# Optimization experiments

Measured on AMD Instinct MI355X. Metric: run time of the kernel, lower is better.

## Reference

```python
import jax, jax.numpy as jnp
import numpy as np

DIM = 2048
K_DIM = 2048
Q_HEADS = 16
KV_HEADS = 4
HEAD_DIM = DIM // Q_HEADS  # 128
KV_DIM = HEAD_DIM * KV_HEADS  # 512
MAX_LEN = 2048
ROPE_THETA = 10000.0
ROPE_FACTOR = 8.0


def _rope_cos_sin(seq_len):
    # Faithful to generate_sin_cos_pos_emb with is_causal=True
    d = HEAD_DIM
    seq_eff = max(seq_len, MAX_LEN)
    base_adj = (ROPE_FACTOR * seq_eff / MAX_LEN - (ROPE_FACTOR - 1.0)) ** (d / (d - 2))
    adjusted_base = ROPE_THETA * base_adj
    inv_freq = 1.0 / adjusted_base ** (np.arange(0, d, 2, dtype=np.float32) / d)
    pos = np.arange(seq_len, dtype=np.float32)  # causal: no centering
    freqs = pos[:, None] * inv_freq[None, :]            # [S, d/2]
    emb = np.concatenate([freqs, freqs], axis=-1)        # [S, d]
    return jnp.asarray(np.cos(emb), jnp.float32), jnp.asarray(np.sin(emb), jnp.float32)


def _rotate_half(x):
    x1, x2 = jnp.split(x, 2, axis=-1)
    return jnp.concatenate([-x2, x1], axis=-1)


def setup_inputs() -> dict:
    key = jax.random.key(0)
    ks = jax.random.split(key, 12)
    B, S = 1, 2048
    s_in = 1.0 / np.sqrt(DIM)
    s_k = 1.0 / np.sqrt(K_DIM)
    return {
        "query": jax.random.normal(ks[0], (B, S, DIM), jnp.float32),
        "key": jax.random.normal(ks[1], (B, S, K_DIM), jnp.float32),
        "value": jax.random.normal(ks[2], (B, S, K_DIM), jnp.float32),
        "Wq": jax.random.uniform(ks[3], (DIM, DIM), jnp.float32, -s_in, s_in),
        "bq": jax.random.uniform(ks[4], (DIM,), jnp.float32, -s_in, s_in),
        "Wk": jax.random.uniform(ks[5], (KV_DIM, K_DIM), jnp.float32, -s_k, s_k),
        "bk": jax.random.uniform(ks[6], (KV_DIM,), jnp.float32, -s_k, s_k),
        "Wv": jax.random.uniform(ks[7], (KV_DIM, K_DIM), jnp.float32, -s_k, s_k),
        "bv": jax.random.uniform(ks[8], (KV_DIM,), jnp.float32, -s_k, s_k),
        "Wo": jax.random.uniform(ks[9], (DIM, DIM), jnp.float32, -s_in, s_in),
        "bo": jax.random.uniform(ks[10], (DIM,), jnp.float32, -s_in, s_in),
    }


def reference(query, key, value, Wq, bq, Wk, bk, Wv, bv, Wo, bo):
    B, S, _ = query.shape
    scale = HEAD_DIM ** -0.5

    q = query @ Wq.T + bq                                   # [B,S,DIM]
    k = key @ Wk.T + bk                                     # [B,S,KV_DIM]
    v = value @ Wv.T + bv                                   # [B,S,KV_DIM]

    q = q.reshape(B, S, Q_HEADS, HEAD_DIM)
    k = k.reshape(B, S, KV_HEADS, HEAD_DIM)
    v = v.reshape(B, S, KV_HEADS, HEAD_DIM)

    cos, sin = _rope_cos_sin(S)                              # [S,D]
    cos = cos[None, :, None, :]
    sin = sin[None, :, None, :]
    q = q * cos + _rotate_half(q) * sin
    k = k * cos + _rotate_half(k) * sin

    # [B,H,S,D]
    q = q.transpose(0, 2, 1, 3)
    k = k.transpose(0, 2, 1, 3)
    v = v.transpose(0, 2, 1, 3)

    rep = Q_HEADS // KV_HEADS
    k = jnp.repeat(k, rep, axis=1)
    v = jnp.repeat(v, rep, axis=1)

    scores = jnp.einsum('bhqd,bhkd->bhqk', q, k) * scale
    causal = jnp.tril(jnp.ones((S, S), bool))
    scores = jnp.where(causal[None, None], scores, jnp.finfo(scores.dtype).min)
    attn = jax.nn.softmax(scores, axis=-1)
    out = jnp.einsum('bhqk,bhkd->bhqd', attn, v)             # [B,H,S,D]

    out = out.transpose(0, 2, 1, 3).reshape(B, S, DIM)
    return out @ Wo.T + bo
```

## Files before the change

kernel.cpp:

```cpp
#include <hip/hip_runtime.h>
#include <stdint.h>

typedef __attribute__((ext_vector_type(8))) short short8;
typedef __attribute__((ext_vector_type(4))) float f32x4;
typedef __attribute__((ext_vector_type(4))) unsigned short u16x4;
typedef unsigned short bf16_t;

__device__ __forceinline__ bf16_t f2bf(float f) {
  union { float f; uint32_t u; } x; x.f = f;
  uint32_t r = x.u + 0x7fffu + ((x.u >> 16) & 1u);
  return (bf16_t)(r >> 16);
}

__device__ __forceinline__ void ld_g2l_16(const bf16_t* g, bf16_t* l) {
  __builtin_amdgcn_global_load_lds(
      (const __attribute__((address_space(1))) void*)g,
      (__attribute__((address_space(3))) void*)l, 16, 0, 0);
}

__global__ void rope_tab(float* __restrict__ CS, float* __restrict__ SN) {
  int idx = blockIdx.x * 256 + threadIdx.x;
  int i = idx & 63, pos = idx >> 6;
  float ang = (float)pos * exp2f((float)i * -0.2076205059f);
  CS[idx] = cosf(ang);
  SN[idx] = sinf(ang);
}

__global__ void convert_all(const float* __restrict__ s0, const float* __restrict__ s1,
                            const float* __restrict__ s2, const float* __restrict__ s3,
                            const float* __restrict__ s4, const float* __restrict__ s5,
                            const float* __restrict__ s6,
                            bf16_t* __restrict__ d0, bf16_t* __restrict__ d1,
                            bf16_t* __restrict__ d2, bf16_t* __restrict__ d3,
                            bf16_t* __restrict__ d4, bf16_t* __restrict__ d5,
                            bf16_t* __restrict__ d6) {
  int i = blockIdx.x * 256 + threadIdx.x;
  const float* src; bf16_t* dst; int off;
  if (i < 5 * 1048576) {
    int t = i >> 20; off = i & 1048575;
    if (t == 0)      { src = s0; dst = d0; }
    else if (t == 1) { src = s1; dst = d1; }
    else if (t == 2) { src = s2; dst = d2; }
    else if (t == 3) { src = s3; dst = d3; }
    else             { src = s4; dst = d4; }
  } else {
    int j = i - 5 * 1048576;
    if (j < 262144) { src = s5; dst = d5; off = j; }
    else            { src = s6; dst = d6; off = j - 262144; }
  }
  f32x4 v = *(const f32x4*)(src + (size_t)off * 4);
  u16x4 o;
  o[0] = f2bf(v[0]); o[1] = f2bf(v[1]); o[2] = f2bf(v[2]); o[3] = f2bf(v[3]);
  *(u16x4*)(dst + (size_t)off * 4) = o;
}

template <int MODE>
__device__ __forceinline__ void gemm_core(
    bf16_t* __restrict__ As, bf16_t* __restrict__ Bs,
    const bf16_t* __restrict__ A, const bf16_t* __restrict__ Bm,
    const float* __restrict__ bias, void* __restrict__ Cout,
    int N, int K, int m0, int n0,
    const float* __restrict__ CS, const float* __restrict__ SN) {
  const int tid = threadIdx.x;
  const int lane = tid & 63, quad = lane >> 4, l16 = lane & 15;
  const int wv = tid >> 6;
  const int m_off = wv * 32;
  const int c0 = tid, c1 = tid + 256;
  const int r0 = c0 >> 2, col0 = (c0 & 3) * 8;
  const int r1 = c1 >> 2, col1 = (c1 & 3) * 8;

  f32x4 acc[2][8];
  const f32x4 zf = {0.f, 0.f, 0.f, 0.f};
#pragma unroll
  for (int mi = 0; mi < 2; ++mi)
#pragma unroll
    for (int ni = 0; ni < 8; ++ni) acc[mi][ni] = zf;

  const bf16_t* Ap0 = A + (size_t)(m0 + r0) * K + col0;
  const bf16_t* Ap1 = A + (size_t)(m0 + r1) * K + col1;
  const bf16_t* Bp0 = Bm + (size_t)(n0 + r0) * K + col0;
  const bf16_t* Bp1 = Bm + (size_t)(n0 + r1) * K + col1;
  bf16_t* lA0 = As + c0 * 8;  bf16_t* lA1 = As + c1 * 8;
  bf16_t* lB0 = Bs + c0 * 8;  bf16_t* lB1 = Bs + c1 * 8;

  for (int k0 = 0; k0 < K; k0 += 32) {
    ld_g2l_16(Ap0 + k0, lA0);
    ld_g2l_16(Ap1 + k0, lA1);
    ld_g2l_16(Bp0 + k0, lB0);
    ld_g2l_16(Bp1 + k0, lB1);
    __syncthreads();
    short8 af[2], bf[8];
#pragma unroll
    for (int mi = 0; mi < 2; ++mi)
      af[mi] = *(const short8*)(&As[(m_off + mi * 16 + l16) * 32 + quad * 8]);
#pragma unroll
    for (int ni = 0; ni < 8; ++ni)
      bf[ni] = *(const short8*)(&Bs[(ni * 16 + l16) * 32 + quad * 8]);
#pragma unroll
    for (int mi = 0; mi < 2; ++mi)
#pragma unroll
      for (int ni = 0; ni < 8; ++ni)
        acc[mi][ni] = __builtin_amdgcn_mfma_f32_16x16x32_bf16(
            af[mi], bf[ni], acc[mi][ni], 0, 0, 0);
    __syncthreads();
  }

  if (MODE == 0 || MODE == 2) {
#pragma unroll
    for (int mi = 0; mi < 2; ++mi)
#pragma unroll
      for (int ni = 0; ni < 8; ++ni) {
        int n = n0 + ni * 16 + l16;
        int mbase = m0 + m_off + mi * 16 + quad * 4;
        float bv = bias[n];
#pragma unroll
        for (int r = 0; r < 4; ++r) {
          float v = acc[mi][ni][r] + bv;
          int m = mbase + r;
          if (MODE == 0) ((float*)Cout)[(size_t)m * N + n] = v;
          else           ((bf16_t*)Cout)[(size_t)n * 2048 + m] = f2bf(v);
        }
      }
  } else {
    const float scale = (MODE == 3) ? 0.08838834764831845f : 1.0f;
    bf16_t* dst = (bf16_t*)Cout;
#pragma unroll
    for (int mi = 0; mi < 2; ++mi)
#pragma unroll
      for (int r = 0; r < 4; ++r) {
        int m = m0 + m_off + mi * 16 + quad * 4 + r;
#pragma unroll
        for (int ni = 0; ni < 4; ++ni) {
          int i = ni * 16 + l16;
          int n_lo = n0 + i;
          float v1 = acc[mi][ni][r] + bias[n_lo];
          float v2 = acc[mi][ni + 4][r] + bias[n_lo + 64];
          float c = CS[m * 64 + i];
          float s = SN[m * 64 + i];
          float o1 = (v1 * c - v2 * s) * scale;
          float o2 = (v2 * c + v1 * s) * scale;
          dst[(size_t)m * N + n_lo] = f2bf(o1);
          dst[(size_t)m * N + n_lo + 64] = f2bf(o2);
        }
      }
  }
}

__global__ __launch_bounds__(256) void gemm_qkv(
    const bf16_t* __restrict__ qb, const bf16_t* __restrict__ kb,
    const bf16_t* __restrict__ vb, const bf16_t* __restrict__ wqb,
    const bf16_t* __restrict__ wkb, const bf16_t* __restrict__ wvb,
    const float* __restrict__ bq, const float* __restrict__ bk,
    const float* __restrict__ bv, bf16_t* __restrict__ Qr,
    bf16_t* __restrict__ Kr, bf16_t* __restrict__ Vt,
    const float* __restrict__ CS, const float* __restrict__ SN) {
  __shared__ __align__(16) bf16_t As[128 * 32];
  __shared__ __align__(16) bf16_t Bs[128 * 32];
  int bx = blockIdx.x, m0 = blockIdx.y * 128;
  if (bx < 16)
    gemm_core<3>(As, Bs, qb, wqb, bq, Qr, 2048, 2048, m0, bx * 128, CS, SN);
  else if (bx < 20)
    gemm_core<4>(As, Bs, kb, wkb, bk, Kr, 512, 2048, m0, (bx - 16) * 128, CS, SN);
  else
    gemm_core<2>(As, Bs, vb, wvb, bv, Vt, 512, 2048, m0, (bx - 20) * 128, CS, SN);
}

__global__ __launch_bounds__(256) void gemm_o(
    const bf16_t* __restrict__ Ob, const bf16_t* __restrict__ wob,
    const float* __restrict__ bo, float* __restrict__ out) {
  __shared__ __align__(16) bf16_t As[128 * 32];
  __shared__ __align__(16) bf16_t Bs[128 * 32];
  gemm_core<0>(As, Bs, Ob, wob, bo, out, 2048, 2048,
               blockIdx.y * 128, blockIdx.x * 128, nullptr, nullptr);
}

__global__ __launch_bounds__(256, 2) void attn_fwd(
    const bf16_t* __restrict__ Qr, const bf16_t* __restrict__ Kr,
    const bf16_t* __restrict__ Vt, bf16_t* __restrict__ Oo) {
  const int h = blockIdx.y;
  const int qt = 31 - blockIdx.x;
  const int tid = threadIdx.x;
  const int wv = tid >> 6, lane = tid & 63, quad = lane >> 4, l16 = lane & 15;
  const int q_base = qt * 64 + wv * 16;
  const int hkv = h >> 2;
  const int qg = q_base + l16;

  __shared__ __align__(16) bf16_t Ks[64 * 136];
  __shared__ __align__(16) bf16_t Vs[128 * 72];
  __shared__ __align__(16) float Sb[4][16 * 66];
  float* mys = Sb[wv];

  short8 qf[4];
  {
    const bf16_t* qp = Qr + (size_t)(q_base + l16) * 2048 + h * 128 + quad * 8;
#pragma unroll
    for (int kc = 0; kc < 4; ++kc) qf[kc] = *(const short8*)(qp + kc * 32);
  }

  const f32x4 zf = {0.f, 0.f, 0.f, 0.f};
  f32x4 o[8];
#pragma unroll
  for (int di = 0; di < 8; ++di) o[di] = zf;
  float l_acc = 0.f;

  const int ntiles = qt + 1;
  for (int t = 0; t < ntiles; ++t) {
    const int k0 = t * 64;
#pragma unroll
    for (int j = 0; j < 4; ++j) {
      int cid = tid + j * 256;
      int row = cid >> 4, c = cid & 15;
      f32x4 tmp = *(const f32x4*)(&Kr[(size_t)(k0 + row) * 512 + hkv * 128 + c * 8]);
      *(f32x4*)(&Ks[row * 136 + c * 8]) = tmp;
    }
#pragma unroll
    for (int j = 0; j < 4; ++j) {
      int cid = tid + j * 256;
      int row = cid >> 3, c = cid & 7;
      f32x4 tmp = *(const f32x4*)(&Vt[(size_t)(hkv * 128 + row) * 2048 + k0 + c * 8]);
      *(f32x4*)(&Vs[row * 72 + c * 8]) = tmp;
    }
    __syncthreads();

    f32x4 sacc[4];
#pragma unroll
    for (int sub = 0; sub < 4; ++sub) sacc[sub] = zf;
#pragma unroll
    for (int sub = 0; sub < 4; ++sub)
#pragma unroll
      for (int kc = 0; kc < 4; ++kc) {
        short8 kf = *(const short8*)(&Ks[(sub * 16 + l16) * 136 + kc * 32 + quad * 8]);
        sacc[sub] = __builtin_amdgcn_mfma_f32_16x16x32_bf16(qf[kc], kf, sacc[sub], 0, 0, 0);
      }
#pragma unroll
    for (int sub = 0; sub < 4; ++sub)
#pragma unroll
      for (int r = 0; r < 4; ++r)
        mys[(quad * 4 + r) * 66 + sub * 16 + l16] = sacc[sub][r];
    __asm__ volatile("s_waitcnt lgkmcnt(0)" ::: "memory");
    const float* rp = mys + l16 * 66 + quad * 8;
    float p0[8], p1[8];
    if (k0 + 63 > q_base) {
#pragma unroll
      for (int j = 0; j < 8; ++j) {
        int kg = k0 + quad * 8 + j;
        p0[j] = (kg <= qg) ? __expf(rp[j]) : 0.f;
        p1[j] = (kg + 32 <= qg) ? __expf(rp[32 + j]) : 0.f;
      }
    } else {
#pragma unroll
      for (int j = 0; j < 8; ++j) {
        p0[j] = __expf(rp[j]);
        p1[j] = __expf(rp[32 + j]);
      }
    }
    float ls = 0.f;
#pragma unroll
    for (int j = 0; j < 8; ++j) ls += p0[j] + p1[j];
    l_acc += ls;
    short8 pf0, pf1;
#pragma unroll
    for (int j = 0; j < 8; ++j) {
      pf0[j] = (short)f2bf(p0[j]);
      pf1[j] = (short)f2bf(p1[j]);
    }
#pragma unroll
    for (int di = 0; di < 8; ++di) {
      short8 vf0 = *(const short8*)(&Vs[(di * 16 + l16) * 72 + quad * 8]);
      short8 vf1 = *(const short8*)(&Vs[(di * 16 + l16) * 72 + 32 + quad * 8]);
      o[di] = __builtin_amdgcn_mfma_f32_16x16x32_bf16(pf0, vf0, o[di], 0, 0, 0);
      o[di] = __builtin_amdgcn_mfma_f32_16x16x32_bf16(pf1, vf1, o[di], 0, 0, 0);
    }
    __syncthreads();
  }

  float lf = l_acc;
  lf += __shfl_xor(lf, 16);
  lf += __shfl_xor(lf, 32);
  float linv[4];
#pragma unroll
  for (int r = 0; r < 4; ++r) linv[r] = 1.0f / __shfl(lf, quad * 4 + r, 64);
#pragma unroll
  for (int di = 0; di < 8; ++di)
#pragma unroll
    for (int r = 0; r < 4; ++r) {
      size_t row = q_base + quad * 4 + r;
      size_t col = h * 128 + di * 16 + l16;
      Oo[row * 2048 + col] = f2bf(o[di][r] * linv[r]);
    }
}

extern "C" void kernel_launch(void* const* d_in, const int* in_sizes, int n_in,
                              void* d_out, int out_size, void* d_ws, size_t ws_size,
                              hipStream_t stream) {
  (void)in_sizes; (void)n_in; (void)out_size; (void)ws_size;
  const float* query = (const float*)d_in[0];
  const float* key = (const float*)d_in[1];
  const float* value = (const float*)d_in[2];
  const float* Wq = (const float*)d_in[3];
  const float* bq = (const float*)d_in[4];
  const float* Wk = (const float*)d_in[5];
  const float* bk = (const float*)d_in[6];
  const float* Wv = (const float*)d_in[7];
  const float* bv = (const float*)d_in[8];
  const float* Wo = (const float*)d_in[9];
  const float* bo = (const float*)d_in[10];
  float* out = (float*)d_out;

  char* ws = (char*)d_ws;
  const size_t MB = 1024 * 1024;
  bf16_t* qb  = (bf16_t*)(ws + 0 * MB);
  bf16_t* kb  = (bf16_t*)(ws + 8 * MB);
  bf16_t* vb  = (bf16_t*)(ws + 16 * MB);
  bf16_t* wqb = (bf16_t*)(ws + 24 * MB);
  bf16_t* wkb = (bf16_t*)(ws + 32 * MB);
  bf16_t* wvb = (bf16_t*)(ws + 34 * MB);
  bf16_t* wob = (bf16_t*)(ws + 36 * MB);
  bf16_t* Qr  = (bf16_t*)(ws + 44 * MB);
  bf16_t* Kr  = (bf16_t*)(ws + 52 * MB);
  bf16_t* Vt  = (bf16_t*)(ws + 54 * MB);
  bf16_t* Ob  = (bf16_t*)(ws + 56 * MB);
  float*  CS  = (float*)(ws + 64 * MB);
  float*  SN  = (float*)(ws + 64 * MB + 512 * 1024);

  rope_tab<<<512, 256, 0, stream>>>(CS, SN);
  convert_all<<<22528, 256, 0, stream>>>(query, key, value, Wq, Wo, Wk, Wv,
                                         qb, kb, vb, wqb, wob, wkb, wvb);
  gemm_qkv<<<dim3(24, 16), 256, 0, stream>>>(qb, kb, vb, wqb, wkb, wvb,
                                             bq, bk, bv, Qr, Kr, Vt, CS, SN);
  attn_fwd<<<dim3(32, 16), 256, 0, stream>>>(Qr, Kr, Vt, Ob);
  gemm_o<<<dim3(16, 16), 256, 0, stream>>>(Ob, wob, bo, out);
}
```

Before: 302.8 us.

## Retile GEMMs with swizzled LDS, load V directly to registers, fuse rope table

```diff
diff --git a/kernel.cpp b/kernel.cpp
--- a/kernel.cpp
+++ b/kernel.cpp
@@ -3,6 +3,7 @@
 
 typedef __attribute__((ext_vector_type(8))) short short8;
 typedef __attribute__((ext_vector_type(4))) float f32x4;
+typedef __attribute__((ext_vector_type(2))) float f32x2;
 typedef __attribute__((ext_vector_type(4))) unsigned short u16x4;
 typedef unsigned short bf16_t;
 
@@ -16,14 +17,6 @@
   __builtin_amdgcn_global_load_lds(
       (const __attribute__((address_space(1))) void*)g,
       (__attribute__((address_space(3))) void*)l, 16, 0, 0);
-}
-
-__global__ void rope_tab(float* __restrict__ CS, float* __restrict__ SN) {
-  int idx = blockIdx.x * 256 + threadIdx.x;
-  int i = idx & 63, pos = idx >> 6;
-  float ang = (float)pos * exp2f((float)i * -0.2076205059f);
-  CS[idx] = cosf(ang);
-  SN[idx] = sinf(ang);
 }
 
 __global__ void convert_all(const float* __restrict__ s0, const float* __restrict__ s1,
@@ -33,7 +26,16 @@
                             bf16_t* __restrict__ d0, bf16_t* __restrict__ d1,
                             bf16_t* __restrict__ d2, bf16_t* __restrict__ d3,
                             bf16_t* __restrict__ d4, bf16_t* __restrict__ d5,
-                            bf16_t* __restrict__ d6) {
+                            bf16_t* __restrict__ d6,
+                            float* __restrict__ CS, float* __restrict__ SN) {
+  if (blockIdx.x >= 22528) {
+    int idx = (blockIdx.x - 22528) * 256 + threadIdx.x;
+    int i = idx & 63, pos = idx >> 6;
+    float ang = (float)pos * exp2f((float)i * -0.2076205059f);
+    CS[idx] = cosf(ang);
+    SN[idx] = sinf(ang);
+    return;
+  }
   int i = blockIdx.x * 256 + threadIdx.x;
   const float* src; bf16_t* dst; int off;
   if (i < 5 * 1048576) {
@@ -64,85 +66,81 @@
   const int tid = threadIdx.x;
   const int lane = tid & 63, quad = lane >> 4, l16 = lane & 15;
   const int wv = tid >> 6;
-  const int m_off = wv * 32;
-  const int c0 = tid, c1 = tid + 256;
-  const int r0 = c0 >> 2, col0 = (c0 & 3) * 8;
-  const int r1 = c1 >> 2, col1 = (c1 & 3) * 8;
-
-  f32x4 acc[2][8];
+
+  const bf16_t* gsrc[6];
+  bf16_t* ldst[6];
+#pragma unroll
+  for (int r = 0; r < 6; ++r) {
+    int s = r * 256 + tid;
+    if (s < 512) {
+      int row = s >> 3, cc = (s & 7) ^ (row & 7);
+      gsrc[r] = A + (size_t)(m0 + row) * K + cc * 8;
+      ldst[r] = As + s * 8;
+    } else {
+      int sb = s - 512;
+      int row = sb >> 3, cc = (sb & 7) ^ (row & 7);
+      gsrc[r] = Bm + (size_t)(n0 + row) * K + cc * 8;
+      ldst[r] = Bs + sb * 8;
+    }
+  }
+
+  f32x4 acc[8];
   const f32x4 zf = {0.f, 0.f, 0.f, 0.f};
 #pragma unroll
-  for (int mi = 0; mi < 2; ++mi)
-#pragma unroll
-    for (int ni = 0; ni < 8; ++ni) acc[mi][ni] = zf;
-
-  const bf16_t* Ap0 = A + (size_t)(m0 + r0) * K + col0;
-  const bf16_t* Ap1 = A + (size_t)(m0 + r1) * K + col1;
-  const bf16_t* Bp0 = Bm + (size_t)(n0 + r0) * K + col0;
-  const bf16_t* Bp1 = Bm + (size_t)(n0 + r1) * K + col1;
-  bf16_t* lA0 = As + c0 * 8;  bf16_t* lA1 = As + c1 * 8;
-  bf16_t* lB0 = Bs + c0 * 8;  bf16_t* lB1 = Bs + c1 * 8;
-
-  for (int k0 = 0; k0 < K; k0 += 32) {
-    ld_g2l_16(Ap0 + k0, lA0);
-    ld_g2l_16(Ap1 + k0, lA1);
-    ld_g2l_16(Bp0 + k0, lB0);
-    ld_g2l_16(Bp1 + k0, lB1);
+  for (int ni = 0; ni < 8; ++ni) acc[ni] = zf;
+
+  for (int k0 = 0; k0 < K; k0 += 64) {
+#pragma unroll
+    for (int r = 0; r < 6; ++r) ld_g2l_16(gsrc[r] + k0, ldst[r]);
     __syncthreads();
-    short8 af[2], bf[8];
-#pragma unroll
-    for (int mi = 0; mi < 2; ++mi)
-      af[mi] = *(const short8*)(&As[(m_off + mi * 16 + l16) * 32 + quad * 8]);
-#pragma unroll
-    for (int ni = 0; ni < 8; ++ni)
-      bf[ni] = *(const short8*)(&Bs[(ni * 16 + l16) * 32 + quad * 8]);
-#pragma unroll
-    for (int mi = 0; mi < 2; ++mi)
-#pragma unroll
-      for (int ni = 0; ni < 8; ++ni)
-        acc[mi][ni] = __builtin_amdgcn_mfma_f32_16x16x32_bf16(
-            af[mi], bf[ni], acc[mi][ni], 0, 0, 0);
+#pragma unroll
+    for (int ks = 0; ks < 2; ++ks) {
+      const int ch = ((ks * 4 + quad) ^ (l16 & 7)) * 8;
+      short8 af = *(const short8*)(&As[(wv * 16 + l16) * 64 + ch]);
+#pragma unroll
+      for (int ni = 0; ni < 8; ++ni) {
+        short8 bf = *(const short8*)(&Bs[(ni * 16 + l16) * 64 + ch]);
+        acc[ni] = __builtin_amdgcn_mfma_f32_16x16x32_bf16(af, bf, acc[ni], 0, 0, 0);
+      }
+    }
     __syncthreads();
   }
 
   if (MODE == 0 || MODE == 2) {
 #pragma unroll
-    for (int mi = 0; mi < 2; ++mi)
-#pragma unroll
-      for (int ni = 0; ni < 8; ++ni) {
-        int n = n0 + ni * 16 + l16;
-        int mbase = m0 + m_off + mi * 16 + quad * 4;
-        float bv = bias[n];
-#pragma unroll
-        for (int r = 0; r < 4; ++r) {
-          float v = acc[mi][ni][r] + bv;
-          int m = mbase + r;
-          if (MODE == 0) ((float*)Cout)[(size_t)m * N + n] = v;
-          else           ((bf16_t*)Cout)[(size_t)n * 2048 + m] = f2bf(v);
-        }
-      }
+    for (int ni = 0; ni < 8; ++ni) {
+      int n = n0 + ni * 16 + l16;
+      int mbase = m0 + wv * 16 + quad * 4;
+      float bv = bias[n];
+      if (MODE == 0) {
+#pragma unroll
+        for (int r = 0; r < 4; ++r)
+          ((float*)Cout)[(size_t)(mbase + r) * N + n] = acc[ni][r] + bv;
+      } else {
+        u16x4 pk;
+#pragma unroll
+        for (int r = 0; r < 4; ++r) pk[r] = f2bf(acc[ni][r] + bv);
+        *(u16x4*)(&((bf16_t*)Cout)[(size_t)n * 2048 + mbase]) = pk;
+      }
+    }
   } else {
     const float scale = (MODE == 3) ? 0.08838834764831845f : 1.0f;
     bf16_t* dst = (bf16_t*)Cout;
 #pragma unroll
-    for (int mi = 0; mi < 2; ++mi)
-#pragma unroll
-      for (int r = 0; r < 4; ++r) {
-        int m = m0 + m_off + mi * 16 + quad * 4 + r;
-#pragma unroll
-        for (int ni = 0; ni < 4; ++ni) {
-          int i = ni * 16 + l16;
-          int n_lo = n0 + i;
-          float v1 = acc[mi][ni][r] + bias[n_lo];
-          float v2 = acc[mi][ni + 4][r] + bias[n_lo + 64];
-          float c = CS[m * 64 + i];
-          float s = SN[m * 64 + i];
-          float o1 = (v1 * c - v2 * s) * scale;
-          float o2 = (v2 * c + v1 * s) * scale;
-          dst[(size_t)m * N + n_lo] = f2bf(o1);
-          dst[(size_t)m * N + n_lo + 64] = f2bf(o2);
-        }
-      }
+    for (int r = 0; r < 4; ++r) {
+      int m = m0 + wv * 16 + quad * 4 + r;
+#pragma unroll
+      for (int ni = 0; ni < 4; ++ni) {
+        int i = ni * 16 + l16;
+        int n_lo = n0 + i;
+        float v1 = acc[ni][r] + bias[n_lo];
+        float v2 = acc[ni + 4][r] + bias[n_lo + 64];
+        float c = CS[m * 64 + i];
+        float s = SN[m * 64 + i];
+        dst[(size_t)m * N + n_lo] = f2bf((v1 * c - v2 * s) * scale);
+        dst[(size_t)m * N + n_lo + 64] = f2bf((v2 * c + v1 * s) * scale);
+      }
+    }
   }
 }
 
@@ -154,9 +152,9 @@
     const float* __restrict__ bv, bf16_t* __restrict__ Qr,
     bf16_t* __restrict__ Kr, bf16_t* __restrict__ Vt,
     const float* __restrict__ CS, const float* __restrict__ SN) {
-  __shared__ __align__(16) bf16_t As[128 * 32];
-  __shared__ __align__(16) bf16_t Bs[128 * 32];
-  int bx = blockIdx.x, m0 = blockIdx.y * 128;
+  __shared__ __align__(16) bf16_t As[64 * 64];
+  __shared__ __align__(16) bf16_t Bs[128 * 64];
+  int bx = blockIdx.x, m0 = blockIdx.y * 64;
   if (bx < 16)
     gemm_core<3>(As, Bs, qb, wqb, bq, Qr, 2048, 2048, m0, bx * 128, CS, SN);
   else if (bx < 20)
@@ -168,10 +166,10 @@
 __global__ __launch_bounds__(256) void gemm_o(
     const bf16_t* __restrict__ Ob, const bf16_t* __restrict__ wob,
     const float* __restrict__ bo, float* __restrict__ out) {
-  __shared__ __align__(16) bf16_t As[128 * 32];
-  __shared__ __align__(16) bf16_t Bs[128 * 32];
+  __shared__ __align__(16) bf16_t As[64 * 64];
+  __shared__ __align__(16) bf16_t Bs[128 * 64];
   gemm_core<0>(As, Bs, Ob, wob, bo, out, 2048, 2048,
-               blockIdx.y * 128, blockIdx.x * 128, nullptr, nullptr);
+               blockIdx.y * 64, blockIdx.x * 128, nullptr, nullptr);
 }
 
 __global__ __launch_bounds__(256, 2) void attn_fwd(
@@ -186,9 +184,8 @@
   const int qg = q_base + l16;
 
   __shared__ __align__(16) bf16_t Ks[64 * 136];
-  __shared__ __align__(16) bf16_t Vs[128 * 72];
-  __shared__ __align__(16) float Sb[4][16 * 66];
-  float* mys = Sb[wv];
+  __shared__ __align__(16) float ST[4][64 * 18];
+  float* myst = ST[wv];
 
   short8 qf[4];
   {
@@ -213,12 +210,15 @@
       f32x4 tmp = *(const f32x4*)(&Kr[(size_t)(k0 + row) * 512 + hkv * 128 + c * 8]);
       *(f32x4*)(&Ks[row * 136 + c * 8]) = tmp;
     }
-#pragma unroll
-    for (int j = 0; j < 4; ++j) {
-      int cid = tid + j * 256;
-      int row = cid >> 3, c = cid & 7;
-      f32x4 tmp = *(const f32x4*)(&Vt[(size_t)(hkv * 128 + row) * 2048 + k0 + c * 8]);
-      *(f32x4*)(&Vs[row * 72 + c * 8]) = tmp;
+    short8 vf0[8], vf1[8];
+    {
+      const bf16_t* vpb = Vt + (size_t)(hkv * 128 + l16) * 2048 + k0 + quad * 8;
+#pragma unroll
+      for (int di = 0; di < 8; ++di) {
+        const bf16_t* vp = vpb + (size_t)(di * 16) * 2048;
+        vf0[di] = *(const short8*)vp;
+        vf1[di] = *(const short8*)(vp + 32);
+      }
     }
     __syncthreads();
 
@@ -235,23 +235,26 @@
 #pragma unroll
     for (int sub = 0; sub < 4; ++sub)
 #pragma unroll
-      for (int r = 0; r < 4; ++r)
-        mys[(quad * 4 + r) * 66 + sub * 16 + l16] = sacc[sub][r];
+      for (int hh = 0; hh < 2; ++hh) {
+        f32x2 v2 = {sacc[sub][2 * hh], sacc[sub][2 * hh + 1]};
+        *(f32x2*)(&myst[(sub * 16 + l16) * 18 + quad * 4 + hh * 2]) = v2;
+      }
     __asm__ volatile("s_waitcnt lgkmcnt(0)" ::: "memory");
-    const float* rp = mys + l16 * 66 + quad * 8;
     float p0[8], p1[8];
     if (k0 + 63 > q_base) {
 #pragma unroll
       for (int j = 0; j < 8; ++j) {
         int kg = k0 + quad * 8 + j;
-        p0[j] = (kg <= qg) ? __expf(rp[j]) : 0.f;
-        p1[j] = (kg + 32 <= qg) ? __expf(rp[32 + j]) : 0.f;
+        float s0 = myst[(quad * 8 + j) * 18 + l16];
+        float s1 = myst[(quad * 8 + j + 32) * 18 + l16];
+        p0[j] = (kg <= qg) ? __expf(s0) : 0.f;
+        p1[j] = (kg + 32 <= qg) ? __expf(s1) : 0.f;
       }
     } else {
 #pragma unroll
       for (int j = 0; j < 8; ++j) {
-        p0[j] = __expf(rp[j]);
-        p1[j] = __expf(rp[32 + j]);
+        p0[j] = __expf(myst[(quad * 8 + j) * 18 + l16]);
+        p1[j] = __expf(myst[(quad * 8 + j + 32) * 18 + l16]);
       }
     }
     float ls = 0.f;
@@ -266,10 +269,8 @@
     }
 #pragma unroll
     for (int di = 0; di < 8; ++di) {
-      short8 vf0 = *(const short8*)(&Vs[(di * 16 + l16) * 72 + quad * 8]);
-      short8 vf1 = *(const short8*)(&Vs[(di * 16 + l16) * 72 + 32 + quad * 8]);
-      o[di] = __builtin_amdgcn_mfma_f32_16x16x32_bf16(pf0, vf0, o[di], 0, 0, 0);
-      o[di] = __builtin_amdgcn_mfma_f32_16x16x32_bf16(pf1, vf1, o[di], 0, 0, 0);
+      o[di] = __builtin_amdgcn_mfma_f32_16x16x32_bf16(vf0[di], pf0, o[di], 0, 0, 0);
+      o[di] = __builtin_amdgcn_mfma_f32_16x16x32_bf16(vf1[di], pf1, o[di], 0, 0, 0);
     }
     __syncthreads();
   }
@@ -277,17 +278,15 @@
   float lf = l_acc;
   lf += __shfl_xor(lf, 16);
   lf += __shfl_xor(lf, 32);
-  float linv[4];
-#pragma unroll
-  for (int r = 0; r < 4; ++r) linv[r] = 1.0f / __shfl(lf, quad * 4 + r, 64);
-#pragma unroll
-  for (int di = 0; di < 8; ++di)
-#pragma unroll
-    for (int r = 0; r < 4; ++r) {
-      size_t row = q_base + quad * 4 + r;
-      size_t col = h * 128 + di * 16 + l16;
-      Oo[row * 2048 + col] = f2bf(o[di][r] * linv[r]);
-    }
+  float linv = 1.0f / lf;
+  const size_t rowb = (size_t)(q_base + l16) * 2048 + h * 128;
+#pragma unroll
+  for (int di = 0; di < 8; ++di) {
+    u16x4 pk;
+#pragma unroll
+    for (int r = 0; r < 4; ++r) pk[r] = f2bf(o[di][r] * linv);
+    *(u16x4*)(&Oo[rowb + di * 16 + quad * 4]) = pk;
+  }
 }
 
 extern "C" void kernel_launch(void* const* d_in, const int* in_sizes, int n_in,
@@ -323,11 +322,10 @@
   float*  CS  = (float*)(ws + 64 * MB);
   float*  SN  = (float*)(ws + 64 * MB + 512 * 1024);
 
-  rope_tab<<<512, 256, 0, stream>>>(CS, SN);
-  convert_all<<<22528, 256, 0, stream>>>(query, key, value, Wq, Wo, Wk, Wv,
-                                         qb, kb, vb, wqb, wob, wkb, wvb);
-  gemm_qkv<<<dim3(24, 16), 256, 0, stream>>>(qb, kb, vb, wqb, wkb, wvb,
+  convert_all<<<23040, 256, 0, stream>>>(query, key, value, Wq, Wo, Wk, Wv,
+                                         qb, kb, vb, wqb, wob, wkb, wvb, CS, SN);
+  gemm_qkv<<<dim3(24, 32), 256, 0, stream>>>(qb, kb, vb, wqb, wkb, wvb,
                                              bq, bk, bv, Qr, Kr, Vt, CS, SN);
   attn_fwd<<<dim3(32, 16), 256, 0, stream>>>(Qr, Kr, Vt, Ob);
-  gemm_o<<<dim3(16, 16), 256, 0, stream>>>(Ob, wob, bo, out);
-}
+  gemm_o<<<dim3(16, 32), 256, 0, stream>>>(Ob, wob, bo, out);
+}
```

Result: slower. 354.8 us (+17.2%).
